# Performance work log

Hardware: AMD Instinct MI355X
Metric: run time of the kernel (lower is better)

The kernel has to match this reference:

```python
import jax, jax.numpy as jnp
import numpy as np

K, T, F = 12000, 35, 7          # voxels, points-per-voxel (cfg.VOXEL_POINT_COUNT), point feature dim
B, D, H, W = 1, 10, 400, 352    # scatter grid: [batch, depth, cfg.INPUT_HEIGHT, cfg.INPUT_WIDTH]
C_OUT = 128
EPS = 1e-3                      # Keras BatchNormalization default epsilon


def setup_inputs() -> dict:
    key = jax.random.key(0)
    ks = jax.random.split(key, 20)
    # point features, with per-voxel padding (points beyond count are zero)
    feat = jax.random.normal(ks[0], (K, T, F), dtype=jnp.float32)
    counts = jax.random.randint(ks[1], (K,), 1, T + 1)
    valid = (jnp.arange(T)[None, :] < counts[:, None]).astype(jnp.float32)  # [K,T]
    feat = feat * valid[:, :, None]
    # voxel coordinates: (batch, d, h, w), in-range per dimension
    c0 = jax.random.randint(ks[2], (K,), 0, B)
    c1 = jax.random.randint(ks[3], (K,), 0, D)
    c2 = jax.random.randint(ks[4], (K,), 0, H)
    c3 = jax.random.randint(ks[5], (K,), 0, W)
    coordinate = jnp.stack([c0, c1, c2, c3], axis=1).astype(jnp.int32)  # [K,4]
    p = lambda i, shape: jax.random.normal(ks[i], shape, dtype=jnp.float32) * 0.1
    return {
        "input_feature": feat,
        "w1": p(6, (F, 16)), "b1": p(7, (16,)),
        "gamma1": 1.0 + p(8, (16,)), "beta1": p(9, (16,)),
        "mean1": p(10, (16,)), "var1": jax.random.uniform(ks[11], (16,), minval=0.5, maxval=1.5),
        "w2": p(12, (32, 64)), "b2": p(13, (64,)),
        "gamma2": 1.0 + p(14, (64,)), "beta2": p(15, (64,)),
        "mean2": p(16, (64,)), "var2": jax.random.uniform(ks[17], (64,), minval=0.5, maxval=1.5),
        "coordinate": coordinate,
        "batch_size": B,
    }


def vfe(x, mask, w, b, gamma, beta, mean, var):
    # Dense + relu (per point), inference BatchNorm, max-aggregate, tile-concat, mask
    dense = jax.nn.relu(jnp.einsum('ktf,fu->ktu', x, w) + b)
    pw = gamma * (dense - mean) * jax.lax.rsqrt(var + EPS) + beta  # [K,T,U]
    agg = jnp.max(pw, axis=1, keepdims=True)                       # [K,1,U]
    cat = jnp.concatenate([pw, jnp.broadcast_to(agg, pw.shape)], axis=2)  # [K,T,2U]
    return cat * mask


def reference(input_feature, w1, b1, gamma1, beta1, mean1, var1,
              w2, b2, gamma2, beta2, mean2, var2, coordinate, batch_size):
    # mask: point is valid if max over its features != 0
    mask = (jnp.max(input_feature, axis=2, keepdims=True) != 0).astype(input_feature.dtype)
    x = vfe(input_feature, mask, w1, b1, gamma1, beta1, mean1, var1)   # [K,T,32]
    x = vfe(x, mask, w2, b2, gamma2, beta2, mean2, var2)               # [K,T,128]
    voxelwise = jnp.max(x, axis=1)                                     # [K,128]
    out = jnp.zeros((batch_size, D, H, W, C_OUT), dtype=voxelwise.dtype)
    # tf.scatter_nd semantics: duplicate indices accumulate (add)
    out = out.at[coordinate[:, 0], coordinate[:, 1], coordinate[:, 2], coordinate[:, 3]].add(voxelwise)
    return out
```

## Files before the change

kernel.cpp:

```cpp
#include <hip/hip_runtime.h>

#define KVOX 12000
#define TPTS 35
#define FIN  7
#define DD   10
#define HH   400
#define WW   352
#define CO   128
#define EPSBN 1e-3f
#define NCELL (DD * HH * WW)
#define TOTALF4 ((size_t)NCELL * 32)
#define FILLB 2048
#define CB    3000

static_assert(CB * 4 == KVOX, "grid covers voxels exactly");

__global__ __launch_bounds__(256) void fill_out(float4* __restrict__ o4)
{
    const float4 z = make_float4(0.f, 0.f, 0.f, 0.f);
    const size_t stride = (size_t)FILLB * 256;
    for (size_t i = (size_t)blockIdx.x * 256 + threadIdx.x; i < TOTALF4; i += stride)
        o4[i] = z;
}

__global__ __launch_bounds__(256) void vfe_scatter(
    const float* __restrict__ feat,
    const float* __restrict__ w1, const float* __restrict__ b1,
    const float* __restrict__ g1, const float* __restrict__ be1,
    const float* __restrict__ m1, const float* __restrict__ v1,
    const float* __restrict__ w2, const float* __restrict__ b2,
    const float* __restrict__ g2, const float* __restrict__ be2,
    const float* __restrict__ m2, const float* __restrict__ v2,
    const int* __restrict__ coord,
    float* __restrict__ out)
{
    const int tid  = threadIdx.x;
    const int wv   = tid >> 6;
    const int lane = tid & 63;
    const int k    = blockIdx.x * 4 + wv;

    __shared__ __align__(16) float sxp[4][TPTS][8];
    __shared__ __align__(16) float spwm[4][TPTS][16];
    __shared__ __align__(16) float sagg[4][16];

    const float* fk = feat + (size_t)k * (TPTS * FIN);

    for (int i = lane; i < TPTS * FIN; i += 64)
        sxp[wv][i / FIN][i % FIN] = fk[i];
    if (lane < TPTS) sxp[wv][lane][FIN] = 0.0f;

    bool pred = false;
    if (lane < TPTS) {
        const float* row = fk + lane * FIN;
        float mx = row[0];
        #pragma unroll
        for (int f = 1; f < FIN; ++f) mx = fmaxf(mx, row[f]);
        pred = (mx != 0.0f);
    }
    const unsigned long long bal = __ballot(pred);
    const int nvalid = __popcll(bal);
    __syncthreads();

    if (lane < 16) {
        const int u = lane;
        float w1c[8];
        #pragma unroll
        for (int f = 0; f < FIN; ++f) w1c[f] = w1[f * 16 + u];
        w1c[FIN] = 0.0f;
        const float b     = b1[u];
        const float scale = g1[u] * rsqrtf(v1[u] + EPSBN);
        const float shift = be1[u] - m1[u] * scale;

        float agg = -INFINITY;
        float pw[TPTS];
        #pragma unroll
        for (int t = 0; t < TPTS; ++t) {
            const float4 xa = *(const float4*)&sxp[wv][t][0];
            const float4 xb = *(const float4*)&sxp[wv][t][4];
            float d = b;
            d = fmaf(xa.x, w1c[0], d); d = fmaf(xa.y, w1c[1], d);
            d = fmaf(xa.z, w1c[2], d); d = fmaf(xa.w, w1c[3], d);
            d = fmaf(xb.x, w1c[4], d); d = fmaf(xb.y, w1c[5], d);
            d = fmaf(xb.z, w1c[6], d); d = fmaf(xb.w, w1c[7], d);
            d = fmaxf(d, 0.0f);
            const float p = fmaf(d, scale, shift);
            agg = fmaxf(agg, p);
            pw[t] = p;
        }
        sagg[wv][u] = agg;
        #pragma unroll
        for (int t = 0; t < TPTS; ++t) {
            const float mk = ((bal >> t) & 1ULL) ? 1.0f : 0.0f;
            spwm[wv][t][u] = pw[t] * mk;
        }
    }
    __syncthreads();

    {
        const int v = lane;
        float w2c[32];
        #pragma unroll
        for (int u = 0; u < 32; ++u) w2c[u] = w2[u * 64 + v];
        const float b     = b2[v];
        const float scale = g2[v] * rsqrtf(v2[v] + EPSBN);
        const float shift = be2[v] - m2[v] * scale;

        float aggdot = 0.0f;
        {
            const float4* ar = (const float4*)&sagg[wv][0];
            #pragma unroll
            for (int q = 0; q < 4; ++q) {
                const float4 a = ar[q];
                aggdot = fmaf(a.x, w2c[16 + 4 * q + 0], aggdot);
                aggdot = fmaf(a.y, w2c[16 + 4 * q + 1], aggdot);
                aggdot = fmaf(a.z, w2c[16 + 4 * q + 2], aggdot);
                aggdot = fmaf(a.w, w2c[16 + 4 * q + 3], aggdot);
            }
        }

        float aggAll = -INFINITY;
        float voxA   = -INFINITY;
        #pragma unroll 7
        for (int t = 0; t < TPTS; ++t) {
            const float mk = ((bal >> t) & 1ULL) ? 1.0f : 0.0f;
            const float4* xr = (const float4*)&spwm[wv][t][0];
            float d = fmaf(mk, aggdot, b);
            #pragma unroll
            for (int q = 0; q < 4; ++q) {
                const float4 xv = xr[q];
                d = fmaf(xv.x, w2c[4 * q + 0], d);
                d = fmaf(xv.y, w2c[4 * q + 1], d);
                d = fmaf(xv.z, w2c[4 * q + 2], d);
                d = fmaf(xv.w, w2c[4 * q + 3], d);
            }
            d = fmaxf(d, 0.0f);
            const float p = fmaf(d, scale, shift);
            aggAll = fmaxf(aggAll, p);
            voxA   = fmaxf(voxA, p * mk);
        }
        float voxB;
        if (nvalid == 0)          voxB = 0.0f;
        else if (nvalid < TPTS)   voxB = fmaxf(aggAll, 0.0f);
        else                      voxB = aggAll;

        const int4 c = ((const int4*)coord)[k];
        const int loc = (((c.x * DD + c.y) * HH + c.z) * WW + c.w);
        float* o = out + (size_t)loc * CO;
        atomicAdd(o + v,      voxA);
        atomicAdd(o + 64 + v, voxB);
    }
}

extern "C" void kernel_launch(void* const* d_in, const int* in_sizes, int n_in,
                              void* d_out, int out_size, void* d_ws, size_t ws_size,
                              hipStream_t stream) {
    const float* feat = (const float*)d_in[0];
    const float* w1   = (const float*)d_in[1];
    const float* b1   = (const float*)d_in[2];
    const float* g1   = (const float*)d_in[3];
    const float* be1  = (const float*)d_in[4];
    const float* m1   = (const float*)d_in[5];
    const float* v1   = (const float*)d_in[6];
    const float* w2   = (const float*)d_in[7];
    const float* b2   = (const float*)d_in[8];
    const float* g2   = (const float*)d_in[9];
    const float* be2  = (const float*)d_in[10];
    const float* m2   = (const float*)d_in[11];
    const float* v2   = (const float*)d_in[12];
    const int*   coord = (const int*)d_in[13];
    float* out = (float*)d_out;

    fill_out<<<FILLB, 256, 0, stream>>>((float4*)out);
    vfe_scatter<<<CB, 256, 0, stream>>>(feat, w1, b1, g1, be1, m1, v1,
                                        w2, b2, g2, be2, m2, v2, coord, out);
}
```

Before: 791.4 us.

## Fuse zero-fill and VFE compute into one cooperative kernel with grid sync

Replaces the separate fill and compute launches with a single cooperative kernel of 1000 blocks. Each block first zero-fills its share of the output, then each wave computes three voxels and holds their results in registers. After a grid-wide sync, every wave performs its scatter atomics. The aim is to overlap the bandwidth-bound zero-fill with the VFE compute and to remove one kernel launch. The cost is a grid barrier and occupancy limited to what a cooperative launch allows. The intra-wave __syncthreads calls were also removed, and the old two-kernel path is kept as a fallback if the cooperative launch fails.

```diff
diff --git a/kernel.cpp b/kernel.cpp
--- a/kernel.cpp
+++ b/kernel.cpp
@@ -1,4 +1,7 @@
 #include <hip/hip_runtime.h>
+#include <hip/hip_cooperative_groups.h>
+
+namespace cg = cooperative_groups;
 
 #define KVOX 12000
 #define TPTS 35
@@ -10,10 +13,167 @@
 #define EPSBN 1e-3f
 #define NCELL (DD * HH * WW)
 #define TOTALF4 ((size_t)NCELL * 32)
+
+#define CGRID 1000
+#define NWAVE (CGRID * 4)
+#define VPW   (KVOX / NWAVE)
+#define F4PT  (TOTALF4 / ((size_t)CGRID * 256))
+
+static_assert(KVOX % NWAVE == 0, "uniform voxels per wave");
+static_assert(TOTALF4 % ((size_t)CGRID * 256) == 0, "uniform fill per thread");
+
 #define FILLB 2048
 #define CB    3000
-
-static_assert(CB * 4 == KVOX, "grid covers voxels exactly");
+static_assert(CB * 4 == KVOX, "fallback grid covers voxels exactly");
+
+__global__ __launch_bounds__(256, 4) void vfe_coop(
+    const float* __restrict__ feat,
+    const float* __restrict__ w1, const float* __restrict__ b1,
+    const float* __restrict__ g1, const float* __restrict__ be1,
+    const float* __restrict__ m1, const float* __restrict__ v1,
+    const float* __restrict__ w2, const float* __restrict__ b2,
+    const float* __restrict__ g2, const float* __restrict__ be2,
+    const float* __restrict__ m2, const float* __restrict__ v2,
+    const int* __restrict__ coord,
+    float* __restrict__ out)
+{
+    const int tid   = threadIdx.x;
+    const int wv    = tid >> 6;
+    const int lane  = tid & 63;
+    const int wslot = blockIdx.x * 4 + wv;
+
+    __shared__ __align__(16) float sxp[4][TPTS][8];
+    __shared__ __align__(16) float spwm[4][TPTS][16];
+    __shared__ __align__(16) float sagg[4][16];
+
+    {
+        const float4 z = make_float4(0.f, 0.f, 0.f, 0.f);
+        float4* o4 = (float4*)out;
+        const size_t base = (size_t)blockIdx.x * 256 + tid;
+        #pragma unroll 8
+        for (int i = 0; i < (int)F4PT; ++i)
+            o4[base + (size_t)i * (CGRID * 256)] = z;
+    }
+
+    float resA[VPW], resB[VPW];
+    int   locs[VPW];
+
+    for (int it = 0; it < VPW; ++it) {
+        const int k = wslot + it * NWAVE;
+        const float* fk = feat + (size_t)k * (TPTS * FIN);
+
+        for (int i = lane; i < TPTS * FIN; i += 64)
+            sxp[wv][i / FIN][i % FIN] = fk[i];
+        if (lane < TPTS) sxp[wv][lane][FIN] = 0.0f;
+
+        bool pred = false;
+        if (lane < TPTS) {
+            const float* row = fk + lane * FIN;
+            float mx = row[0];
+            #pragma unroll
+            for (int f = 1; f < FIN; ++f) mx = fmaxf(mx, row[f]);
+            pred = (mx != 0.0f);
+        }
+        const unsigned long long bal = __ballot(pred);
+        const int nvalid = __popcll(bal);
+
+        if (lane < 16) {
+            const int u = lane;
+            float w1c[8];
+            #pragma unroll
+            for (int f = 0; f < FIN; ++f) w1c[f] = w1[f * 16 + u];
+            w1c[FIN] = 0.0f;
+            const float b     = b1[u];
+            const float scale = g1[u] * rsqrtf(v1[u] + EPSBN);
+            const float shift = be1[u] - m1[u] * scale;
+
+            float agg = -INFINITY;
+            float pw[TPTS];
+            #pragma unroll
+            for (int t = 0; t < TPTS; ++t) {
+                const float4 xa = *(const float4*)&sxp[wv][t][0];
+                const float4 xb = *(const float4*)&sxp[wv][t][4];
+                float d = b;
+                d = fmaf(xa.x, w1c[0], d); d = fmaf(xa.y, w1c[1], d);
+                d = fmaf(xa.z, w1c[2], d); d = fmaf(xa.w, w1c[3], d);
+                d = fmaf(xb.x, w1c[4], d); d = fmaf(xb.y, w1c[5], d);
+                d = fmaf(xb.z, w1c[6], d); d = fmaf(xb.w, w1c[7], d);
+                d = fmaxf(d, 0.0f);
+                const float p = fmaf(d, scale, shift);
+                agg = fmaxf(agg, p);
+                pw[t] = p;
+            }
+            sagg[wv][u] = agg;
+            #pragma unroll
+            for (int t = 0; t < TPTS; ++t) {
+                const float mk = ((bal >> t) & 1ULL) ? 1.0f : 0.0f;
+                spwm[wv][t][u] = pw[t] * mk;
+            }
+        }
+
+        {
+            const int v = lane;
+            float w2c[32];
+            #pragma unroll
+            for (int u = 0; u < 32; ++u) w2c[u] = w2[u * 64 + v];
+            const float b     = b2[v];
+            const float scale = g2[v] * rsqrtf(v2[v] + EPSBN);
+            const float shift = be2[v] - m2[v] * scale;
+
+            float aggdot = 0.0f;
+            {
+                const float4* ar = (const float4*)&sagg[wv][0];
+                #pragma unroll
+                for (int q = 0; q < 4; ++q) {
+                    const float4 a = ar[q];
+                    aggdot = fmaf(a.x, w2c[16 + 4 * q + 0], aggdot);
+                    aggdot = fmaf(a.y, w2c[16 + 4 * q + 1], aggdot);
+                    aggdot = fmaf(a.z, w2c[16 + 4 * q + 2], aggdot);
+                    aggdot = fmaf(a.w, w2c[16 + 4 * q + 3], aggdot);
+                }
+            }
+
+            float aggAll = -INFINITY;
+            float voxA   = -INFINITY;
+            #pragma unroll 7
+            for (int t = 0; t < TPTS; ++t) {
+                const float mk = ((bal >> t) & 1ULL) ? 1.0f : 0.0f;
+                const float4* xr = (const float4*)&spwm[wv][t][0];
+                float d = fmaf(mk, aggdot, b);
+                #pragma unroll
+                for (int q = 0; q < 4; ++q) {
+                    const float4 xv = xr[q];
+                    d = fmaf(xv.x, w2c[4 * q + 0], d);
+                    d = fmaf(xv.y, w2c[4 * q + 1], d);
+                    d = fmaf(xv.z, w2c[4 * q + 2], d);
+                    d = fmaf(xv.w, w2c[4 * q + 3], d);
+                }
+                d = fmaxf(d, 0.0f);
+                const float p = fmaf(d, scale, shift);
+                aggAll = fmaxf(aggAll, p);
+                voxA   = fmaxf(voxA, p * mk);
+            }
+            float voxB;
+            if (nvalid == 0)          voxB = 0.0f;
+            else if (nvalid < TPTS)   voxB = fmaxf(aggAll, 0.0f);
+            else                      voxB = aggAll;
+
+            const int4 c = ((const int4*)coord)[k];
+            locs[it] = (((c.x * DD + c.y) * HH + c.z) * WW + c.w);
+            resA[it] = voxA;
+            resB[it] = voxB;
+        }
+    }
+
+    cg::this_grid().sync();
+
+    #pragma unroll
+    for (int it = 0; it < VPW; ++it) {
+        float* o = out + (size_t)locs[it] * CO;
+        atomicAdd(o + lane,      resA[it]);
+        atomicAdd(o + 64 + lane, resB[it]);
+    }
+}
 
 __global__ __launch_bounds__(256) void fill_out(float4* __restrict__ o4)
 {
@@ -161,6 +321,7 @@
     const float* be1  = (const float*)d_in[4];
     const float* m1   = (const float*)d_in[5];
     const float* v1   = (const float*)d_in[6];
+    const float* v1g  = nullptr; (void)v1g;
     const float* w2   = (const float*)d_in[7];
     const float* b2   = (const float*)d_in[8];
     const float* g2   = (const float*)d_in[9];
@@ -170,7 +331,18 @@
     const int*   coord = (const int*)d_in[13];
     float* out = (float*)d_out;
 
-    fill_out<<<FILLB, 256, 0, stream>>>((float4*)out);
-    vfe_scatter<<<CB, 256, 0, stream>>>(feat, w1, b1, g1, be1, m1, v1,
-                                        w2, b2, g2, be2, m2, v2, coord, out);
+    void* args[] = {
+        (void*)&feat,
+        (void*)&w1, (void*)&b1, (void*)&g1, (void*)&be1, (void*)&m1, (void*)&v1,
+        (void*)&w2, (void*)&b2, (void*)&g2, (void*)&be2, (void*)&m2, (void*)&v2,
+        (void*)&coord, (void*)&out
+    };
+    hipError_t err = hipLaunchCooperativeKernel((const void*)vfe_coop,
+                                                dim3(CGRID), dim3(256),
+                                                args, 0, stream);
+    if (err != hipSuccess) {
+        fill_out<<<FILLB, 256, 0, stream>>>((float4*)out);
+        vfe_scatter<<<CB, 256, 0, stream>>>(feat, w1, b1, g1, be1, m1, v1,
+                                            w2, b2, g2, be2, m2, v2, coord, out);
+    }
 }
```

New measurement: 921.6 us. +16.4%, slower.

## Claim output cells via mark buffer and zero only unclaimed background

Applied to the files above, without the earlier changes.

Replaces the full zero-fill followed by atomicAdd scatter with four passes. A workspace mark array is cleared, then voxels claim their cell with atomicCAS and write their features with plain stores. A background pass zeroes every cell that is unclaimed or claimed more than once, and a fix-up pass recomputes and atomically adds the features of voxels that share a cell. The aim is to avoid atomic read-modify-write traffic and to skip re-zeroing claimed cells. In exchange it adds extra launches, a per-element mark read in the background pass, and repeated VFE work for duplicate cells, while the background zeroing still writes almost the whole output.

```diff
diff --git a/kernel.cpp b/kernel.cpp
--- a/kernel.cpp
+++ b/kernel.cpp
@@ -10,10 +10,227 @@
 #define EPSBN 1e-3f
 #define NCELL (DD * HH * WW)
 #define TOTALF4 ((size_t)NCELL * 32)
+#define MULTI 0xFFFFFFFFu
+#define MARKB ((size_t)NCELL * 4)
+#define MARKF4 (NCELL / 4)
+
+#define CLRB  512
+#define CB    3000
+#define WRB   2048
 #define FILLB 2048
-#define CB    3000
 
 static_assert(CB * 4 == KVOX, "grid covers voxels exactly");
+static_assert(NCELL % 4 == 0, "mark region float4-clearable");
+
+__device__ __forceinline__ void vfe_wave(
+    int k, int wv, int lane,
+    const float* __restrict__ feat,
+    const float* __restrict__ w1, const float* __restrict__ b1,
+    const float* __restrict__ g1, const float* __restrict__ be1,
+    const float* __restrict__ m1, const float* __restrict__ v1,
+    const float* __restrict__ w2, const float* __restrict__ b2,
+    const float* __restrict__ g2, const float* __restrict__ be2,
+    const float* __restrict__ m2, const float* __restrict__ v2,
+    float (&sxp)[TPTS][8], float (&spwm)[TPTS][16], float (&sagg)[16],
+    float& voxA_out, float& voxB_out)
+{
+    const float* fk = feat + (size_t)k * (TPTS * FIN);
+
+    for (int i = lane; i < TPTS * FIN; i += 64)
+        sxp[i / FIN][i % FIN] = fk[i];
+    if (lane < TPTS) sxp[lane][FIN] = 0.0f;
+
+    bool pred = false;
+    if (lane < TPTS) {
+        const float* row = fk + lane * FIN;
+        float mx = row[0];
+        #pragma unroll
+        for (int f = 1; f < FIN; ++f) mx = fmaxf(mx, row[f]);
+        pred = (mx != 0.0f);
+    }
+    const unsigned long long bal = __ballot(pred);
+    const int nvalid = __popcll(bal);
+
+    if (lane < 16) {
+        const int u = lane;
+        float w1c[8];
+        #pragma unroll
+        for (int f = 0; f < FIN; ++f) w1c[f] = w1[f * 16 + u];
+        w1c[FIN] = 0.0f;
+        const float b     = b1[u];
+        const float scale = g1[u] * rsqrtf(v1[u] + EPSBN);
+        const float shift = be1[u] - m1[u] * scale;
+
+        float agg = -INFINITY;
+        float pw[TPTS];
+        #pragma unroll
+        for (int t = 0; t < TPTS; ++t) {
+            const float4 xa = *(const float4*)&sxp[t][0];
+            const float4 xb = *(const float4*)&sxp[t][4];
+            float d = b;
+            d = fmaf(xa.x, w1c[0], d); d = fmaf(xa.y, w1c[1], d);
+            d = fmaf(xa.z, w1c[2], d); d = fmaf(xa.w, w1c[3], d);
+            d = fmaf(xb.x, w1c[4], d); d = fmaf(xb.y, w1c[5], d);
+            d = fmaf(xb.z, w1c[6], d); d = fmaf(xb.w, w1c[7], d);
+            d = fmaxf(d, 0.0f);
+            const float p = fmaf(d, scale, shift);
+            agg = fmaxf(agg, p);
+            pw[t] = p;
+        }
+        sagg[u] = agg;
+        #pragma unroll
+        for (int t = 0; t < TPTS; ++t) {
+            const float mk = ((bal >> t) & 1ULL) ? 1.0f : 0.0f;
+            spwm[t][u] = pw[t] * mk;
+        }
+    }
+
+    const int v = lane;
+    float w2c[32];
+    #pragma unroll
+    for (int u = 0; u < 32; ++u) w2c[u] = w2[u * 64 + v];
+    const float b     = b2[v];
+    const float scale = g2[v] * rsqrtf(v2[v] + EPSBN);
+    const float shift = be2[v] - m2[v] * scale;
+
+    float aggdot = 0.0f;
+    {
+        const float4* ar = (const float4*)&sagg[0];
+        #pragma unroll
+        for (int q = 0; q < 4; ++q) {
+            const float4 a = ar[q];
+            aggdot = fmaf(a.x, w2c[16 + 4 * q + 0], aggdot);
+            aggdot = fmaf(a.y, w2c[16 + 4 * q + 1], aggdot);
+            aggdot = fmaf(a.z, w2c[16 + 4 * q + 2], aggdot);
+            aggdot = fmaf(a.w, w2c[16 + 4 * q + 3], aggdot);
+        }
+    }
+
+    float aggAll = -INFINITY;
+    float voxA   = -INFINITY;
+    #pragma unroll 7
+    for (int t = 0; t < TPTS; ++t) {
+        const float mk = ((bal >> t) & 1ULL) ? 1.0f : 0.0f;
+        const float4* xr = (const float4*)&spwm[t][0];
+        float d = fmaf(mk, aggdot, b);
+        #pragma unroll
+        for (int q = 0; q < 4; ++q) {
+            const float4 xv = xr[q];
+            d = fmaf(xv.x, w2c[4 * q + 0], d);
+            d = fmaf(xv.y, w2c[4 * q + 1], d);
+            d = fmaf(xv.z, w2c[4 * q + 2], d);
+            d = fmaf(xv.w, w2c[4 * q + 3], d);
+        }
+        d = fmaxf(d, 0.0f);
+        const float p = fmaf(d, scale, shift);
+        aggAll = fmaxf(aggAll, p);
+        voxA   = fmaxf(voxA, p * mk);
+    }
+    float voxB;
+    if (nvalid == 0)          voxB = 0.0f;
+    else if (nvalid < TPTS)   voxB = fmaxf(aggAll, 0.0f);
+    else                      voxB = aggAll;
+
+    voxA_out = voxA;
+    voxB_out = voxB;
+}
+
+__global__ __launch_bounds__(256) void clear_marks(float4* __restrict__ m4)
+{
+    const float4 z = make_float4(0.f, 0.f, 0.f, 0.f);
+    const int stride = CLRB * 256;
+    for (int i = blockIdx.x * 256 + threadIdx.x; i < MARKF4; i += stride)
+        m4[i] = z;
+}
+
+__global__ __launch_bounds__(256) void vfe_claim(
+    const float* __restrict__ feat,
+    const float* __restrict__ w1, const float* __restrict__ b1,
+    const float* __restrict__ g1, const float* __restrict__ be1,
+    const float* __restrict__ m1, const float* __restrict__ v1,
+    const float* __restrict__ w2, const float* __restrict__ b2,
+    const float* __restrict__ g2, const float* __restrict__ be2,
+    const float* __restrict__ m2, const float* __restrict__ v2,
+    const int* __restrict__ coord,
+    unsigned* __restrict__ mark,
+    float* __restrict__ out)
+{
+    const int tid  = threadIdx.x;
+    const int wv   = tid >> 6;
+    const int lane = tid & 63;
+    const int k    = blockIdx.x * 4 + wv;
+
+    __shared__ __align__(16) float sxp[4][TPTS][8];
+    __shared__ __align__(16) float spwm[4][TPTS][16];
+    __shared__ __align__(16) float sagg[4][16];
+
+    float voxA, voxB;
+    vfe_wave(k, wv, lane, feat, w1, b1, g1, be1, m1, v1,
+             w2, b2, g2, be2, m2, v2,
+             sxp[wv], spwm[wv], sagg[wv], voxA, voxB);
+
+    const int4 c = ((const int4*)coord)[k];
+    const int loc = (((c.x * DD + c.y) * HH + c.z) * WW + c.w);
+
+    int won = 0;
+    if (lane == 0) {
+        const unsigned old = atomicCAS(mark + loc, 0u, (unsigned)(k + 1));
+        if (old != 0u) atomicExch(mark + loc, MULTI);
+        won = (old == 0u);
+    }
+    won = __shfl(won, 0);
+    if (won) {
+        float* o = out + (size_t)loc * CO;
+        o[lane]      = voxA;
+        o[64 + lane] = voxB;
+    }
+}
+
+__global__ __launch_bounds__(256) void write_bg(
+    const unsigned* __restrict__ mark, float4* __restrict__ out4)
+{
+    const float4 z = make_float4(0.f, 0.f, 0.f, 0.f);
+    const size_t stride = (size_t)WRB * 256;
+    for (size_t i = (size_t)blockIdx.x * 256 + threadIdx.x; i < TOTALF4; i += stride) {
+        const unsigned m = mark[i >> 5];
+        if ((m == 0u) | (m == MULTI)) out4[i] = z;
+    }
+}
+
+__global__ __launch_bounds__(256) void vfe_dupfix(
+    const float* __restrict__ feat,
+    const float* __restrict__ w1, const float* __restrict__ b1,
+    const float* __restrict__ g1, const float* __restrict__ be1,
+    const float* __restrict__ m1, const float* __restrict__ v1,
+    const float* __restrict__ w2, const float* __restrict__ b2,
+    const float* __restrict__ g2, const float* __restrict__ be2,
+    const float* __restrict__ m2, const float* __restrict__ v2,
+    const int* __restrict__ coord,
+    const unsigned* __restrict__ mark,
+    float* __restrict__ out)
+{
+    const int tid  = threadIdx.x;
+    const int wv   = tid >> 6;
+    const int lane = tid & 63;
+    const int k    = blockIdx.x * 4 + wv;
+
+    __shared__ __align__(16) float sxp[4][TPTS][8];
+    __shared__ __align__(16) float spwm[4][TPTS][16];
+    __shared__ __align__(16) float sagg[4][16];
+
+    const int4 c = ((const int4*)coord)[k];
+    const int loc = (((c.x * DD + c.y) * HH + c.z) * WW + c.w);
+    if (mark[loc] != MULTI) return;
+
+    float voxA, voxB;
+    vfe_wave(k, wv, lane, feat, w1, b1, g1, be1, m1, v1,
+             w2, b2, g2, be2, m2, v2,
+             sxp[wv], spwm[wv], sagg[wv], voxA, voxB);
+
+    float* o = out + (size_t)loc * CO;
+    atomicAdd(o + lane,      voxA);
+    atomicAdd(o + 64 + lane, voxB);
+}
 
 __global__ __launch_bounds__(256) void fill_out(float4* __restrict__ o4)
 {
@@ -43,112 +260,16 @@
     __shared__ __align__(16) float spwm[4][TPTS][16];
     __shared__ __align__(16) float sagg[4][16];
 
-    const float* fk = feat + (size_t)k * (TPTS * FIN);
-
-    for (int i = lane; i < TPTS * FIN; i += 64)
-        sxp[wv][i / FIN][i % FIN] = fk[i];
-    if (lane < TPTS) sxp[wv][lane][FIN] = 0.0f;
-
-    bool pred = false;
-    if (lane < TPTS) {
-        const float* row = fk + lane * FIN;
-        float mx = row[0];
-        #pragma unroll
-        for (int f = 1; f < FIN; ++f) mx = fmaxf(mx, row[f]);
-        pred = (mx != 0.0f);
-    }
-    const unsigned long long bal = __ballot(pred);
-    const int nvalid = __popcll(bal);
-    __syncthreads();
-
-    if (lane < 16) {
-        const int u = lane;
-        float w1c[8];
-        #pragma unroll
-        for (int f = 0; f < FIN; ++f) w1c[f] = w1[f * 16 + u];
-        w1c[FIN] = 0.0f;
-        const float b     = b1[u];
-        const float scale = g1[u] * rsqrtf(v1[u] + EPSBN);
-        const float shift = be1[u] - m1[u] * scale;
-
-        float agg = -INFINITY;
-        float pw[TPTS];
-        #pragma unroll
-        for (int t = 0; t < TPTS; ++t) {
-            const float4 xa = *(const float4*)&sxp[wv][t][0];
-            const float4 xb = *(const float4*)&sxp[wv][t][4];
-            float d = b;
-            d = fmaf(xa.x, w1c[0], d); d = fmaf(xa.y, w1c[1], d);
-            d = fmaf(xa.z, w1c[2], d); d = fmaf(xa.w, w1c[3], d);
-            d = fmaf(xb.x, w1c[4], d); d = fmaf(xb.y, w1c[5], d);
-            d = fmaf(xb.z, w1c[6], d); d = fmaf(xb.w, w1c[7], d);
-            d = fmaxf(d, 0.0f);
-            const float p = fmaf(d, scale, shift);
-            agg = fmaxf(agg, p);
-            pw[t] = p;
-        }
-        sagg[wv][u] = agg;
-        #pragma unroll
-        for (int t = 0; t < TPTS; ++t) {
-            const float mk = ((bal >> t) & 1ULL) ? 1.0f : 0.0f;
-            spwm[wv][t][u] = pw[t] * mk;
-        }
-    }
-    __syncthreads();
-
-    {
-        const int v = lane;
-        float w2c[32];
-        #pragma unroll
-        for (int u = 0; u < 32; ++u) w2c[u] = w2[u * 64 + v];
-        const float b     = b2[v];
-        const float scale = g2[v] * rsqrtf(v2[v] + EPSBN);
-        const float shift = be2[v] - m2[v] * scale;
-
-        float aggdot = 0.0f;
-        {
-            const float4* ar = (const float4*)&sagg[wv][0];
-            #pragma unroll
-            for (int q = 0; q < 4; ++q) {
-                const float4 a = ar[q];
-                aggdot = fmaf(a.x, w2c[16 + 4 * q + 0], aggdot);
-                aggdot = fmaf(a.y, w2c[16 + 4 * q + 1], aggdot);
-                aggdot = fmaf(a.z, w2c[16 + 4 * q + 2], aggdot);
-                aggdot = fmaf(a.w, w2c[16 + 4 * q + 3], aggdot);
-            }
-        }
-
-        float aggAll = -INFINITY;
-        float voxA   = -INFINITY;
-        #pragma unroll 7
-        for (int t = 0; t < TPTS; ++t) {
-            const float mk = ((bal >> t) & 1ULL) ? 1.0f : 0.0f;
-            const float4* xr = (const float4*)&spwm[wv][t][0];
-            float d = fmaf(mk, aggdot, b);
-            #pragma unroll
-            for (int q = 0; q < 4; ++q) {
-                const float4 xv = xr[q];
-                d = fmaf(xv.x, w2c[4 * q + 0], d);
-                d = fmaf(xv.y, w2c[4 * q + 1], d);
-                d = fmaf(xv.z, w2c[4 * q + 2], d);
-                d = fmaf(xv.w, w2c[4 * q + 3], d);
-            }
-            d = fmaxf(d, 0.0f);
-            const float p = fmaf(d, scale, shift);
-            aggAll = fmaxf(aggAll, p);
-            voxA   = fmaxf(voxA, p * mk);
-        }
-        float voxB;
-        if (nvalid == 0)          voxB = 0.0f;
-        else if (nvalid < TPTS)   voxB = fmaxf(aggAll, 0.0f);
-        else                      voxB = aggAll;
-
-        const int4 c = ((const int4*)coord)[k];
-        const int loc = (((c.x * DD + c.y) * HH + c.z) * WW + c.w);
-        float* o = out + (size_t)loc * CO;
-        atomicAdd(o + v,      voxA);
-        atomicAdd(o + 64 + v, voxB);
-    }
+    float voxA, voxB;
+    vfe_wave(k, wv, lane, feat, w1, b1, g1, be1, m1, v1,
+             w2, b2, g2, be2, m2, v2,
+             sxp[wv], spwm[wv], sagg[wv], voxA, voxB);
+
+    const int4 c = ((const int4*)coord)[k];
+    const int loc = (((c.x * DD + c.y) * HH + c.z) * WW + c.w);
+    float* o = out + (size_t)loc * CO;
+    atomicAdd(o + lane,      voxA);
+    atomicAdd(o + 64 + lane, voxB);
 }
 
 extern "C" void kernel_launch(void* const* d_in, const int* in_sizes, int n_in,
@@ -170,7 +291,19 @@
     const int*   coord = (const int*)d_in[13];
     float* out = (float*)d_out;
 
-    fill_out<<<FILLB, 256, 0, stream>>>((float4*)out);
-    vfe_scatter<<<CB, 256, 0, stream>>>(feat, w1, b1, g1, be1, m1, v1,
-                                        w2, b2, g2, be2, m2, v2, coord, out);
-}
+    if (ws_size >= MARKB) {
+        unsigned* mark = (unsigned*)d_ws;
+        clear_marks<<<CLRB, 256, 0, stream>>>((float4*)d_ws);
+        vfe_claim<<<CB, 256, 0, stream>>>(feat, w1, b1, g1, be1, m1, v1,
+                                          w2, b2, g2, be2, m2, v2,
+                                          coord, mark, out);
+        write_bg<<<WRB, 256, 0, stream>>>(mark, (float4*)out);
+        vfe_dupfix<<<CB, 256, 0, stream>>>(feat, w1, b1, g1, be1, m1, v1,
+                                           w2, b2, g2, be2, m2, v2,
+                                           coord, mark, out);
+    } else {
+        fill_out<<<FILLB, 256, 0, stream>>>((float4*)out);
+        vfe_scatter<<<CB, 256, 0, stream>>>(feat, w1, b1, g1, be1, m1, v1,
+                                            w2, b2, g2, be2, m2, v2, coord, out);
+    }
+}
```

Measured after the change: 773.0 us. 2.3% less time.
